# Kernel tuning notes

Measured on AMD Instinct MI355X. Metric: run time of the kernel, lower is better.

Reference implementation:

```python
import jax, jax.numpy as jnp
import numpy as np

N = 32768      # total nodes (512 graphs x 64 padded nodes)
E = 262144     # edges (avg degree 8)
F_IN = 74      # atom feature dim
D0 = 128       # dim_embedding
D1 = 256       # hidden feats
B = 512        # batch_size (graphs)
NPG = 64       # nodes per graph
EPS = 1e-5     # BatchNorm1d eps


def setup_inputs() -> dict:
    key = jax.random.key(0)
    ks = jax.random.split(key, 8)
    def rn(k, shape, s=0.05):
        return jax.random.normal(k, shape, jnp.float32) * s
    # init_transform weight [D0, F_IN]; padding=True zeroes the last row
    W_init = rn(ks[0], (D0, F_IN)).at[-1].set(0.0)
    return {
        "node_feats": jax.random.normal(ks[1], (N, F_IN), jnp.float32),
        "W_init": W_init,
        "gcn_w1": rn(ks[2], (D0, D1)), "gcn_b1": jnp.zeros((D1,), jnp.float32),
        "res_w1": rn(ks[3], (D1, D0)), "res_b1": jnp.zeros((D1,), jnp.float32),
        "bn_g1": jnp.ones((D1,), jnp.float32), "bn_b1": jnp.zeros((D1,), jnp.float32),
        "gcn_w2": rn(ks[4], (D1, D1)), "gcn_b2": jnp.zeros((D1,), jnp.float32),
        "bn_g2": jnp.ones((D1,), jnp.float32), "bn_b2": jnp.zeros((D1,), jnp.float32),
        "edge_src": jax.random.randint(ks[5], (E,), 0, N),
        "edge_dst": jax.random.randint(ks[6], (E,), 0, N),
    }


def _agg(x, src, dst):
    # DGL GraphConv norm='both': D_out^{-1/2} gather-scatter D_in^{-1/2}, degrees clamped to >= 1
    ones = jnp.ones((src.shape[0],), x.dtype)
    deg_out = jnp.clip(jax.ops.segment_sum(ones, src, num_segments=N), 1.0)
    deg_in = jnp.clip(jax.ops.segment_sum(ones, dst, num_segments=N), 1.0)
    xs = x * jax.lax.rsqrt(deg_out)[:, None]
    agg = jax.ops.segment_sum(xs[src], dst, num_segments=N)  # [N, d]
    return agg * jax.lax.rsqrt(deg_in)[:, None]


def _bn(x, g, b):
    # BatchNorm1d training-mode: batch stats over node axis, biased var
    m = x.mean(0)
    v = x.var(0)
    return (x - m) * jax.lax.rsqrt(v + EPS) * g + b


def reference(node_feats, W_init, gcn_w1, gcn_b1, res_w1, res_b1, bn_g1, bn_b1,
              gcn_w2, gcn_b2, bn_g2, bn_b2, edge_src, edge_dst):
    h = node_feats @ W_init.T  # [N, D0]
    # layer 1: residual Linear 128->256, GCN(aggregate then weight, since in<out), GELU, BN
    res = h @ res_w1.T + res_b1
    g = jax.nn.gelu(_agg(h, edge_src, edge_dst) @ gcn_w1 + gcn_b1, approximate=False)
    h = _bn(g + res, bn_g1, bn_b1)
    # layer 2: Identity residual
    g = jax.nn.gelu(_agg(h, edge_src, edge_dst) @ gcn_w2 + gcn_b2, approximate=False)
    h = _bn(g + h, bn_g2, bn_b2)
    return h.reshape(B, NPG, D1)
```

## Files before the change

### kernel.cpp

```cpp
#include <hip/hip_runtime.h>
#include <hip/hip_bf16.h>
#include <math.h>

#define N_NODES 32768
#define E_EDGES 262144
#define F_INF   74
#define KP      96
#define D0      128
#define D1      256
#define BN_EPS  1e-5f
#define RBLK    1024

#if __has_builtin(__builtin_amdgcn_cvt_pk_f32_fp8)
#define HW_FP8 1
#else
#define HW_FP8 0
#endif

typedef float f32x4 __attribute__((ext_vector_type(4)));
typedef float f32x2 __attribute__((ext_vector_type(2)));
typedef short s16x8 __attribute__((ext_vector_type(8)));

__device__ __forceinline__ float b2f(ushort h) { return __uint_as_float(((unsigned)h) << 16); }
__device__ __forceinline__ ushort f2b(float f) {
    unsigned u = __float_as_uint(f);
    return (ushort)((u + 0x7FFFu + ((u >> 16) & 1u)) >> 16);
}
__device__ __forceinline__ unsigned char f2q(float f) {
    unsigned u = __float_as_uint(f * 7.52316384526264005e-37f);
    unsigned s = (u >> 24) & 0x80u;
    int r = (int)(((u & 0x7fffffffu) + 0x80000u) >> 20);
    r = r > 126 ? 126 : r;
    return (unsigned char)(s | (unsigned)r);
}
__device__ __forceinline__ float q2f(unsigned x) {
    unsigned fb = ((x & 0x80u) << 24) | ((x & 0x7fu) << 20);
    return __uint_as_float(fb) * 1.32922799578491587e+36f;
}
__device__ __forceinline__ void acc8(float* a, uint2 v, float c) {
#if HW_FP8
    f32x2 p;
    p = __builtin_amdgcn_cvt_pk_f32_fp8((int)v.x, false); a[0] += p[0] * c; a[1] += p[1] * c;
    p = __builtin_amdgcn_cvt_pk_f32_fp8((int)v.x, true);  a[2] += p[0] * c; a[3] += p[1] * c;
    p = __builtin_amdgcn_cvt_pk_f32_fp8((int)v.y, false); a[4] += p[0] * c; a[5] += p[1] * c;
    p = __builtin_amdgcn_cvt_pk_f32_fp8((int)v.y, true);  a[6] += p[0] * c; a[7] += p[1] * c;
#else
    unsigned d;
    d = v.x; a[0] += q2f(d & 255u) * c; a[1] += q2f((d >> 8) & 255u) * c;
             a[2] += q2f((d >> 16) & 255u) * c; a[3] += q2f(d >> 24) * c;
    d = v.y; a[4] += q2f(d & 255u) * c; a[5] += q2f((d >> 8) & 255u) * c;
             a[6] += q2f((d >> 16) & 255u) * c; a[7] += q2f(d >> 24) * c;
#endif
}
__device__ __forceinline__ float gelu_exact(float x) {
    return 0.5f * x * (1.0f + erff(x * 0.70710678118654752440f));
}


__global__ void k_front_a(const int* __restrict__ src, const int* __restrict__ dst,
                          int* __restrict__ deg,
                          const float* __restrict__ nf, const float* __restrict__ Wi,
                          const float* __restrict__ w1, const float* __restrict__ rw,
                          const float* __restrict__ w2,
                          ushort* __restrict__ nfB, ushort* __restrict__ WTB,
                          ushort* __restrict__ WB1, ushort* __restrict__ RWB,
                          ushort* __restrict__ WB2) {
    int bid = blockIdx.x;
    int tid = threadIdx.x;
    if (bid < 1024) {
        int e = bid * 256 + tid;
        atomicAdd(&deg[src[e]], 1);
        atomicAdd(&deg[N_NODES + dst[e]], 1);
        return;
    }
    int idx = (bid - 1024) * 256 + tid;
    {
        int n = idx / KP, k = idx - n * KP;
        nfB[idx] = (k < F_INF) ? f2b(nf[n * F_INF + k]) : (ushort)0;
    }
    if (idx < D0 * KP) {
        int c = idx / KP, k = idx - c * KP;
        WTB[idx] = (k < F_INF) ? f2b(Wi[c * F_INF + k]) : (ushort)0;
    }
    if (idx < D1 * D0) {
        int n = idx >> 7, k = idx & 127;
        WB1[idx] = f2b(w1[k * D1 + n]);
        RWB[idx] = f2b(rw[idx]);
    }
    if (idx < D1 * D1) {
        int n = idx >> 8, k = idx & 255;
        WB2[idx] = f2b(w2[k * D1 + n]);
    }
}

__global__ __launch_bounds__(1024) void k_scan(const int* __restrict__ deg,
                                               int* __restrict__ row_off,
                                               float* __restrict__ rsq_out,
                                               float* __restrict__ rsq_in,
                                               int* __restrict__ cursor) {
    __shared__ int part[1024];
    int t = threadIdx.x;
    int base = t * 32;
    int loc[32];
    int s = 0;
    #pragma unroll
    for (int i = 0; i < 32; i++) { loc[i] = s; s += deg[N_NODES + base + i]; }
    part[t] = s;
    #pragma unroll
    for (int i = 0; i < 32; i++) {
        int n = base + i;
        int d_o = deg[n];           if (d_o < 1) d_o = 1;
        int d_i = deg[N_NODES + n]; if (d_i < 1) d_i = 1;
        rsq_out[n] = 1.0f / sqrtf((float)d_o);
        rsq_in[n]  = 1.0f / sqrtf((float)d_i);
        cursor[n] = 0;
    }
    __syncthreads();
    for (int off = 1; off < 1024; off <<= 1) {
        int v = 0;
        if (t >= off) v = part[t - off];
        __syncthreads();
        if (t >= off) part[t] += v;
        __syncthreads();
    }
    int pre = (t == 0) ? 0 : part[t - 1];
    #pragma unroll
    for (int i = 0; i < 32; i++) row_off[base + i] = pre + loc[i];
    if (t == 1023) row_off[N_NODES] = part[1023];
}


__global__ __launch_bounds__(512) void k_front_b(
    const int* __restrict__ src, const int* __restrict__ dst,
    const int* __restrict__ row_off, const float* __restrict__ rsq_out,
    int* __restrict__ cursor, int2* __restrict__ csr,
    const ushort* __restrict__ nfB, const ushort* __restrict__ WTB,
    ushort* __restrict__ h0) {
    int bid = blockIdx.x;
    int tid = threadIdx.x;
    if (bid < 512) {
        int e = bid * 512 + tid;
        int d = dst[e];
        int s = src[e];
        int slot = atomicAdd(&cursor[d], 1);
        int pos = row_off[d] + slot;
        csr[pos] = make_int2(s, __float_as_int(rsq_out[s]));
        return;
    }
    int b2 = bid - 512;
    int w = tid >> 6, lane = tid & 63, m = lane & 15, g4 = lane >> 4;
    int col = w * 16 + m;
    int rbase = b2 * 16;
    s16x8 B[3], A[3];
    #pragma unroll
    for (int j = 0; j < 3; j++)
        B[j] = *reinterpret_cast<const s16x8*>(&WTB[(size_t)col * KP + j * 32 + g4 * 8]);
    #pragma unroll
    for (int j = 0; j < 3; j++)
        A[j] = *reinterpret_cast<const s16x8*>(&nfB[(size_t)(rbase + m) * KP + j * 32 + g4 * 8]);
    f32x4 acc = (f32x4){0.f, 0.f, 0.f, 0.f};
    #pragma unroll
    for (int j = 0; j < 3; j++)
        acc = __builtin_amdgcn_mfma_f32_16x16x32_bf16(A[j], B[j], acc, 0, 0, 0);
    #pragma unroll
    for (int r = 0; r < 4; r++)
        h0[(size_t)(rbase + g4 * 4 + r) * D0 + col] = f2b(acc[r]);
}


__global__ __launch_bounds__(512) void k_layer1f(
    const ushort* __restrict__ h0B, const float* __restrict__ rsq_in,
    const int* __restrict__ row_off, const int2* __restrict__ csr,
    const ushort* __restrict__ WB1, const ushort* __restrict__ RWB,
    const float* __restrict__ b1, const float* __restrict__ rb,
    ushort* __restrict__ t1B, unsigned char* __restrict__ t1Q,
    float* __restrict__ partials) {
    __shared__ ushort sA[32 * 128];
    int tid = threadIdx.x;
    int rbase = blockIdx.x * 32;
    {
        int nloc = tid >> 4;
        int half = (tid >> 3) & 1;
        int node = rbase + nloc;
        int f = (tid & 7) * 8;
        int beg = row_off[node], end = row_off[node + 1];
        float a0[8], a1[8];
        #pragma unroll
        for (int j = 0; j < 8; j++) { a0[j] = 0.f; a1[j] = 0.f; }
        int e = beg + half;
        for (; e + 6 < end; e += 8) {
            int2 r0 = csr[e], r1 = csr[e + 2], r2 = csr[e + 4], r3 = csr[e + 6];
            float c0 = __int_as_float(r0.y), c1 = __int_as_float(r1.y);
            float c2 = __int_as_float(r2.y), c3 = __int_as_float(r3.y);
            s16x8 v00 = *reinterpret_cast<const s16x8*>(&h0B[(size_t)r0.x * D0 + f]);
            s16x8 v01 = *reinterpret_cast<const s16x8*>(&h0B[(size_t)r0.x * D0 + f + 64]);
            s16x8 v10 = *reinterpret_cast<const s16x8*>(&h0B[(size_t)r1.x * D0 + f]);
            s16x8 v11 = *reinterpret_cast<const s16x8*>(&h0B[(size_t)r1.x * D0 + f + 64]);
            s16x8 v20 = *reinterpret_cast<const s16x8*>(&h0B[(size_t)r2.x * D0 + f]);
            s16x8 v21 = *reinterpret_cast<const s16x8*>(&h0B[(size_t)r2.x * D0 + f + 64]);
            s16x8 v30 = *reinterpret_cast<const s16x8*>(&h0B[(size_t)r3.x * D0 + f]);
            s16x8 v31 = *reinterpret_cast<const s16x8*>(&h0B[(size_t)r3.x * D0 + f + 64]);
            #pragma unroll
            for (int j = 0; j < 8; j++) {
                a0[j] += b2f((ushort)v00[j]) * c0 + b2f((ushort)v10[j]) * c1 +
                         b2f((ushort)v20[j]) * c2 + b2f((ushort)v30[j]) * c3;
                a1[j] += b2f((ushort)v01[j]) * c0 + b2f((ushort)v11[j]) * c1 +
                         b2f((ushort)v21[j]) * c2 + b2f((ushort)v31[j]) * c3;
            }
        }
        for (; e < end; e += 2) {
            int2 r = csr[e];
            float sc = __int_as_float(r.y);
            s16x8 v0 = *reinterpret_cast<const s16x8*>(&h0B[(size_t)r.x * D0 + f]);
            s16x8 v1 = *reinterpret_cast<const s16x8*>(&h0B[(size_t)r.x * D0 + f + 64]);
            #pragma unroll
            for (int j = 0; j < 8; j++) {
                a0[j] += b2f((ushort)v0[j]) * sc;
                a1[j] += b2f((ushort)v1[j]) * sc;
            }
        }
        #pragma unroll
        for (int j = 0; j < 8; j++) {
            a0[j] += __shfl_xor(a0[j], 8);
            a1[j] += __shfl_xor(a1[j], 8);
        }
        if (half == 0) {
            float si = rsq_in[node];
            s16x8 o0, o1;
            #pragma unroll
            for (int j = 0; j < 8; j++) {
                o0[j] = (short)f2b(a0[j] * si);
                o1[j] = (short)f2b(a1[j] * si);
            }
            int swz = (nloc & 15) << 4;
            int x0 = f * 2;
            *reinterpret_cast<s16x8*>(((char*)sA) + nloc * 256 + (x0 ^ swz)) = o0;
            *reinterpret_cast<s16x8*>(((char*)sA) + nloc * 256 + ((x0 + 128) ^ swz)) = o1;
        }
    }
    __syncthreads();
    int w = tid >> 6, lane = tid & 63, m = lane & 15, g4 = lane >> 4;
    int cb = w * 32;
    s16x8 BG[2][4], BR[2][4];
    #pragma unroll
    for (int nt = 0; nt < 2; nt++)
        #pragma unroll
        for (int j = 0; j < 4; j++) {
            BG[nt][j] = *reinterpret_cast<const s16x8*>(&WB1[(size_t)(cb + nt * 16 + m) * D0 + j * 32 + g4 * 8]);
            BR[nt][j] = *reinterpret_cast<const s16x8*>(&RWB[(size_t)(cb + nt * 16 + m) * D0 + j * 32 + g4 * 8]);
        }
    float bg[2], brv[2];
    #pragma unroll
    for (int nt = 0; nt < 2; nt++) {
        bg[nt]  = b1[cb + nt * 16 + m];
        brv[nt] = rb[cb + nt * 16 + m];
    }
    float ps[2] = {0.f, 0.f}, pq[2] = {0.f, 0.f};
    #pragma unroll
    for (int rt = 0; rt < 2; rt++) {
        int row = rt * 16 + m;
        s16x8 aA[4], aH[4];
        #pragma unroll
        for (int j = 0; j < 4; j++) {
            int boff = row * 256 + (((j * 4 + g4) * 16) ^ ((row & 15) << 4));
            aA[j] = *reinterpret_cast<const s16x8*>(((const char*)sA) + boff);
            aH[j] = *reinterpret_cast<const s16x8*>(&h0B[(size_t)(rbase + row) * D0 + j * 32 + g4 * 8]);
        }
        f32x4 accG[2], accR[2];
        #pragma unroll
        for (int nt = 0; nt < 2; nt++) {
            accG[nt] = (f32x4){0.f, 0.f, 0.f, 0.f};
            accR[nt] = (f32x4){0.f, 0.f, 0.f, 0.f};
        }
        #pragma unroll
        for (int j = 0; j < 4; j++)
            #pragma unroll
            for (int nt = 0; nt < 2; nt++) {
                accG[nt] = __builtin_amdgcn_mfma_f32_16x16x32_bf16(aA[j], BG[nt][j], accG[nt], 0, 0, 0);
                accR[nt] = __builtin_amdgcn_mfma_f32_16x16x32_bf16(aH[j], BR[nt][j], accR[nt], 0, 0, 0);
            }
        #pragma unroll
        for (int nt = 0; nt < 2; nt++) {
            int col = cb + nt * 16 + m;
            #pragma unroll
            for (int r = 0; r < 4; r++) {
                int orow = rbase + rt * 16 + g4 * 4 + r;
                float v = gelu_exact(accG[nt][r] + bg[nt]) + accR[nt][r] + brv[nt];
                t1B[(size_t)orow * D1 + col] = f2b(v);
                t1Q[(size_t)orow * D1 + col] = f2q(v);
                ps[nt] += v; pq[nt] += v * v;
            }
        }
    }
    #pragma unroll
    for (int nt = 0; nt < 2; nt++) {
        float s = ps[nt], q = pq[nt];
        s += __shfl_xor(s, 16); s += __shfl_xor(s, 32);
        q += __shfl_xor(q, 16); q += __shfl_xor(q, 32);
        if (g4 == 0) {
            int col = cb + nt * 16 + m;
            partials[(size_t)col * RBLK + blockIdx.x] = s;
            partials[(size_t)(256 + col) * RBLK + blockIdx.x] = q;
        }
    }
}


__global__ __launch_bounds__(1024) void k_layer2f(
    const ushort* __restrict__ t1B, const unsigned char* __restrict__ t1Q,
    const float* __restrict__ sc1, const float* __restrict__ sh1,
    const float* __restrict__ rsq_in,
    const int* __restrict__ row_off, const int2* __restrict__ csr,
    const ushort* __restrict__ WB2, const float* __restrict__ b2,
    ushort* __restrict__ t2B, float* __restrict__ partials) {
    __shared__ ushort sA[32 * 256];
    int tid = threadIdx.x;
    int rbase = blockIdx.x * 32;
    {
        int nloc = tid >> 5;
        int l32 = tid & 31;
        int node = rbase + nloc;
        int f0 = l32 * 8;
        int beg = row_off[node], end = row_off[node + 1];
        int deg = end - beg;
        int grp = (tid & 63) & 32;
        float a[8];
        #pragma unroll
        for (int j = 0; j < 8; j++) a[j] = 0.f;
        float ssum = 0.f;
        int2 my = (l32 < deg) ? csr[beg + l32] : make_int2(0, 0);
        int nb = deg < 32 ? deg : 32;
        for (int kb = 0; kb < nb; kb += 8) {
            int s[8]; float c[8];
            #pragma unroll
            for (int k2 = 0; k2 < 8; k2++) {
                s[k2] = __shfl(my.x, grp + kb + k2);
                c[k2] = __int_as_float(__shfl(my.y, grp + kb + k2));
            }
            uint2 q[8];
            #pragma unroll
            for (int k2 = 0; k2 < 8; k2++)
                q[k2] = *reinterpret_cast<const uint2*>(&t1Q[(size_t)s[k2] * D1 + f0]);
            #pragma unroll
            for (int k2 = 0; k2 < 8; k2++) {
                acc8(a, q[k2], c[k2]);
                ssum += c[k2];
            }
        }
        for (int e = beg + 32; e < end; e++) {
            int2 r = csr[e];
            float sc = __int_as_float(r.y);
            uint2 q = *reinterpret_cast<const uint2*>(&t1Q[(size_t)r.x * D1 + f0]);
            ssum += sc;
            acc8(a, q, sc);
        }
        float si = rsq_in[node];
        s16x8 o;
        #pragma unroll
        for (int j = 0; j < 8; j++)
            o[j] = (short)f2b((sc1[f0 + j] * a[j] + sh1[f0 + j] * ssum) * si);
        int swz = (nloc & 15) << 4;
        int boff = nloc * 512 + ((f0 * 2) ^ swz);
        *reinterpret_cast<s16x8*>(((char*)sA) + boff) = o;
    }
    __syncthreads();
    int w = tid >> 6, lane = tid & 63, m = lane & 15, g4 = lane >> 4;
    int col = w * 16 + m;
    ushort rres[2][4];
    #pragma unroll
    for (int rt = 0; rt < 2; rt++)
        #pragma unroll
        for (int r = 0; r < 4; r++)
            rres[rt][r] = t1B[(size_t)(rbase + rt * 16 + g4 * 4 + r) * D1 + col];
    s16x8 BG[8];
    #pragma unroll
    for (int j = 0; j < 8; j++)
        BG[j] = *reinterpret_cast<const s16x8*>(&WB2[(size_t)col * D1 + j * 32 + g4 * 8]);
    float bg = b2[col], a1c = sc1[col], s1c = sh1[col];
    float ps = 0.f, pq = 0.f;
    #pragma unroll
    for (int rt = 0; rt < 2; rt++) {
        int row = rt * 16 + m;
        s16x8 aA[8];
        #pragma unroll
        for (int j = 0; j < 8; j++) {
            int boff = row * 512 + (((j * 4 + g4) * 16) ^ ((row & 15) << 4));
            aA[j] = *reinterpret_cast<const s16x8*>(((const char*)sA) + boff);
        }
        f32x4 acc = (f32x4){0.f, 0.f, 0.f, 0.f};
        #pragma unroll
        for (int j = 0; j < 8; j++)
            acc = __builtin_amdgcn_mfma_f32_16x16x32_bf16(aA[j], BG[j], acc, 0, 0, 0);
        #pragma unroll
        for (int r = 0; r < 4; r++) {
            int orow = rbase + rt * 16 + g4 * 4 + r;
            float h1v = fmaf(b2f(rres[rt][r]), a1c, s1c);
            float v = gelu_exact(acc[r] + bg) + h1v;
            t2B[(size_t)orow * D1 + col] = f2b(v);
            ps += v; pq += v * v;
        }
    }
    ps += __shfl_xor(ps, 16); ps += __shfl_xor(ps, 32);
    pq += __shfl_xor(pq, 16); pq += __shfl_xor(pq, 32);
    if (g4 == 0) {
        partials[(size_t)col * RBLK + blockIdx.x] = ps;
        partials[(size_t)(256 + col) * RBLK + blockIdx.x] = pq;
    }
}


__global__ __launch_bounds__(256) void k_reduce(
    const float* __restrict__ partials, const float* __restrict__ g,
    const float* __restrict__ b, float* __restrict__ sc, float* __restrict__ sh) {
    int c = blockIdx.x;
    int t = threadIdx.x;
    const float* ps = partials + (size_t)c * RBLK;
    const float* pq = partials + (size_t)(256 + c) * RBLK;
    float s = ps[t] + ps[t + 256] + ps[t + 512] + ps[t + 768];
    float q = pq[t] + pq[t + 256] + pq[t + 512] + pq[t + 768];
    __shared__ float Ls[256], Lq[256];
    Ls[t] = s; Lq[t] = q;
    __syncthreads();
    for (int o = 128; o > 0; o >>= 1) {
        if (t < o) { Ls[t] += Ls[t + o]; Lq[t] += Lq[t + o]; }
        __syncthreads();
    }
    if (t == 0) {
        float m = Ls[0] * (1.0f / (float)N_NODES);
        float var = Lq[0] * (1.0f / (float)N_NODES) - m * m;
        float a = g[c] / sqrtf(var + BN_EPS);
        sc[c] = a;
        sh[c] = b[c] - m * a;
    }
}


__global__ __launch_bounds__(256) void k_apply(
    const ushort* __restrict__ t2B, const float* __restrict__ sc,
    const float* __restrict__ sh, float* __restrict__ out) {
    int idx = blockIdx.x * 256 + threadIdx.x;
    size_t base = (size_t)idx * 8;
    int c = (int)(base & 255);
    s16x8 v = *reinterpret_cast<const s16x8*>(&t2B[base]);
    float4 o0, o1;
    o0.x = fmaf(b2f((ushort)v[0]), sc[c + 0], sh[c + 0]);
    o0.y = fmaf(b2f((ushort)v[1]), sc[c + 1], sh[c + 1]);
    o0.z = fmaf(b2f((ushort)v[2]), sc[c + 2], sh[c + 2]);
    o0.w = fmaf(b2f((ushort)v[3]), sc[c + 3], sh[c + 3]);
    o1.x = fmaf(b2f((ushort)v[4]), sc[c + 4], sh[c + 4]);
    o1.y = fmaf(b2f((ushort)v[5]), sc[c + 5], sh[c + 5]);
    o1.z = fmaf(b2f((ushort)v[6]), sc[c + 6], sh[c + 6]);
    o1.w = fmaf(b2f((ushort)v[7]), sc[c + 7], sh[c + 7]);
    *reinterpret_cast<float4*>(&out[base]) = o0;
    *reinterpret_cast<float4*>(&out[base + 4]) = o1;
}


static inline size_t align256(size_t x) { return (x + 255) & ~(size_t)255; }

extern "C" void kernel_launch(void* const* d_in, const int* in_sizes, int n_in,
                              void* d_out, int out_size, void* d_ws, size_t ws_size,
                              hipStream_t stream) {
    const float* node_feats = (const float*)d_in[0];
    const float* W_init     = (const float*)d_in[1];
    const float* gcn_w1     = (const float*)d_in[2];
    const float* gcn_b1     = (const float*)d_in[3];
    const float* res_w1     = (const float*)d_in[4];
    const float* res_b1     = (const float*)d_in[5];
    const float* bn_g1      = (const float*)d_in[6];
    const float* bn_b1      = (const float*)d_in[7];
    const float* gcn_w2     = (const float*)d_in[8];
    const float* gcn_b2     = (const float*)d_in[9];
    const float* bn_g2      = (const float*)d_in[10];
    const float* bn_b2      = (const float*)d_in[11];
    const int*   edge_src   = (const int*)d_in[12];
    const int*   edge_dst   = (const int*)d_in[13];
    float* out = (float*)d_out;

    char* p = (char*)d_ws;
    size_t off = 0;
    auto take = [&](size_t bytes) { void* r = p + off; off += align256(bytes); return r; };

    ushort* h0B   = (ushort*)take((size_t)N_NODES * D0 * 2);
    ushort* t1B   = (ushort*)take((size_t)N_NODES * D1 * 2);
    unsigned char* t1Q = (unsigned char*)take((size_t)N_NODES * D1);
    ushort* t2B   = (ushort*)take((size_t)N_NODES * D1 * 2);
    ushort* nfB   = (ushort*)take((size_t)N_NODES * KP * 2);
    ushort* WTB   = (ushort*)take((size_t)D0 * KP * 2);
    ushort* WB1   = (ushort*)take((size_t)D1 * D0 * 2);
    ushort* RWB   = (ushort*)take((size_t)D1 * D0 * 2);
    ushort* WB2   = (ushort*)take((size_t)D1 * D1 * 2);
    float*  part1 = (float*)take((size_t)2 * 256 * RBLK * 4);
    float*  part2 = (float*)take((size_t)2 * 256 * RBLK * 4);
    float*  sc1   = (float*)take(256 * 4);
    float*  sh1   = (float*)take(256 * 4);
    float*  sc2   = (float*)take(256 * 4);
    float*  sh2   = (float*)take(256 * 4);
    float*  rsq_out = (float*)take((size_t)N_NODES * 4);
    float*  rsq_in  = (float*)take((size_t)N_NODES * 4);
    int*    degi    = (int*)take((size_t)2 * N_NODES * 4);
    int*    cursor  = (int*)take((size_t)N_NODES * 4);
    int*    row_off = (int*)take((size_t)(N_NODES + 2) * 4);
    int2*   csr     = (int2*)take((size_t)E_EDGES * 8);

    hipMemsetAsync(degi, 0, (size_t)2 * N_NODES * 4, stream);

    k_front_a<<<1024 + (N_NODES * KP) / 256, 256, 0, stream>>>(
        edge_src, edge_dst, degi, node_feats, W_init, gcn_w1, res_w1, gcn_w2,
        nfB, WTB, WB1, RWB, WB2);

    k_scan<<<1, 1024, 0, stream>>>(degi, row_off, rsq_out, rsq_in, cursor);

    k_front_b<<<512 + N_NODES / 16, 512, 0, stream>>>(
        edge_src, edge_dst, row_off, rsq_out, cursor, csr, nfB, WTB, h0B);

    k_layer1f<<<RBLK, 512, 0, stream>>>(h0B, rsq_in, row_off, csr,
                                        WB1, RWB, gcn_b1, res_b1, t1B, t1Q, part1);
    k_reduce<<<256, 256, 0, stream>>>(part1, bn_g1, bn_b1, sc1, sh1);

    k_layer2f<<<RBLK, 1024, 0, stream>>>(t1B, t1Q, sc1, sh1, rsq_in, row_off, csr,
                                         WB2, gcn_b2, t2B, part2);
    k_reduce<<<256, 256, 0, stream>>>(part2, bn_g2, bn_b2, sc2, sh2);

    k_apply<<<(N_NODES * D1 / 8) / 256, 256, 0, stream>>>(t2B, sc2, sh2, out);
}
```

Baseline: 198.9 us.

## Overlap init-transform GEMM with single-block scan; split CSR fill into own kernel

Moves the h0 = node_feats @ W_init^T MFMA work out of the CSR-fill kernel and into the same launch as the single-block prefix scan. The scan runs in block 0 while the other blocks compute h0, 32 rows per 1024-thread block. This is meant to hide the latency of the serial one-block scan behind useful work. The CSR fill becomes its own small kernel, so the launch count stays the same but stage boundaries move.

```diff
diff --git a/kernel.cpp b/kernel.cpp
--- a/kernel.cpp
+++ b/kernel.cpp
@@ -93,64 +93,49 @@
     }
 }
 
-__global__ __launch_bounds__(1024) void k_scan(const int* __restrict__ deg,
-                                               int* __restrict__ row_off,
-                                               float* __restrict__ rsq_out,
-                                               float* __restrict__ rsq_in,
-                                               int* __restrict__ cursor) {
-    __shared__ int part[1024];
-    int t = threadIdx.x;
-    int base = t * 32;
-    int loc[32];
-    int s = 0;
-    #pragma unroll
-    for (int i = 0; i < 32; i++) { loc[i] = s; s += deg[N_NODES + base + i]; }
-    part[t] = s;
-    #pragma unroll
-    for (int i = 0; i < 32; i++) {
-        int n = base + i;
-        int d_o = deg[n];           if (d_o < 1) d_o = 1;
-        int d_i = deg[N_NODES + n]; if (d_i < 1) d_i = 1;
-        rsq_out[n] = 1.0f / sqrtf((float)d_o);
-        rsq_in[n]  = 1.0f / sqrtf((float)d_i);
-        cursor[n] = 0;
-    }
-    __syncthreads();
-    for (int off = 1; off < 1024; off <<= 1) {
-        int v = 0;
-        if (t >= off) v = part[t - off];
-        __syncthreads();
-        if (t >= off) part[t] += v;
-        __syncthreads();
-    }
-    int pre = (t == 0) ? 0 : part[t - 1];
-    #pragma unroll
-    for (int i = 0; i < 32; i++) row_off[base + i] = pre + loc[i];
-    if (t == 1023) row_off[N_NODES] = part[1023];
-}
-
-
-__global__ __launch_bounds__(512) void k_front_b(
-    const int* __restrict__ src, const int* __restrict__ dst,
-    const int* __restrict__ row_off, const float* __restrict__ rsq_out,
-    int* __restrict__ cursor, int2* __restrict__ csr,
+
+__global__ __launch_bounds__(1024) void k_scan_init(
+    const int* __restrict__ deg,
+    int* __restrict__ row_off, float* __restrict__ rsq_out,
+    float* __restrict__ rsq_in, int* __restrict__ cursor,
     const ushort* __restrict__ nfB, const ushort* __restrict__ WTB,
     ushort* __restrict__ h0) {
-    int bid = blockIdx.x;
-    int tid = threadIdx.x;
-    if (bid < 512) {
-        int e = bid * 512 + tid;
-        int d = dst[e];
-        int s = src[e];
-        int slot = atomicAdd(&cursor[d], 1);
-        int pos = row_off[d] + slot;
-        csr[pos] = make_int2(s, __float_as_int(rsq_out[s]));
+    int t = threadIdx.x;
+    if (blockIdx.x == 0) {
+        __shared__ int part[1024];
+        int base = t * 32;
+        int loc[32];
+        int s = 0;
+        #pragma unroll
+        for (int i = 0; i < 32; i++) { loc[i] = s; s += deg[N_NODES + base + i]; }
+        part[t] = s;
+        #pragma unroll
+        for (int i = 0; i < 32; i++) {
+            int n = base + i;
+            int d_o = deg[n];           if (d_o < 1) d_o = 1;
+            int d_i = deg[N_NODES + n]; if (d_i < 1) d_i = 1;
+            rsq_out[n] = 1.0f / sqrtf((float)d_o);
+            rsq_in[n]  = 1.0f / sqrtf((float)d_i);
+            cursor[n] = 0;
+        }
+        __syncthreads();
+        for (int off = 1; off < 1024; off <<= 1) {
+            int v = 0;
+            if (t >= off) v = part[t - off];
+            __syncthreads();
+            if (t >= off) part[t] += v;
+            __syncthreads();
+        }
+        int pre = (t == 0) ? 0 : part[t - 1];
+        #pragma unroll
+        for (int i = 0; i < 32; i++) row_off[base + i] = pre + loc[i];
+        if (t == 1023) row_off[N_NODES] = part[1023];
         return;
     }
-    int b2 = bid - 512;
-    int w = tid >> 6, lane = tid & 63, m = lane & 15, g4 = lane >> 4;
-    int col = w * 16 + m;
-    int rbase = b2 * 16;
+    int b2 = blockIdx.x - 1;
+    int w = t >> 6, lane = t & 63, m = lane & 15, g4 = lane >> 4;
+    int col = (w & 7) * 16 + m;
+    int rbase = b2 * 32 + (w >> 3) * 16;
     s16x8 B[3], A[3];
     #pragma unroll
     for (int j = 0; j < 3; j++)
@@ -165,6 +150,19 @@
     #pragma unroll
     for (int r = 0; r < 4; r++)
         h0[(size_t)(rbase + g4 * 4 + r) * D0 + col] = f2b(acc[r]);
+}
+
+
+__global__ __launch_bounds__(512) void k_fill(
+    const int* __restrict__ src, const int* __restrict__ dst,
+    const int* __restrict__ row_off, const float* __restrict__ rsq_out,
+    int* __restrict__ cursor, int2* __restrict__ csr) {
+    int e = blockIdx.x * 512 + threadIdx.x;
+    int d = dst[e];
+    int s = src[e];
+    int slot = atomicAdd(&cursor[d], 1);
+    int pos = row_off[d] + slot;
+    csr[pos] = make_int2(s, __float_as_int(rsq_out[s]));
 }
 
 
@@ -509,10 +507,11 @@
         edge_src, edge_dst, degi, node_feats, W_init, gcn_w1, res_w1, gcn_w2,
         nfB, WTB, WB1, RWB, WB2);
 
-    k_scan<<<1, 1024, 0, stream>>>(degi, row_off, rsq_out, rsq_in, cursor);
-
-    k_front_b<<<512 + N_NODES / 16, 512, 0, stream>>>(
-        edge_src, edge_dst, row_off, rsq_out, cursor, csr, nfB, WTB, h0B);
+    k_scan_init<<<1 + N_NODES / 32, 1024, 0, stream>>>(
+        degi, row_off, rsq_out, rsq_in, cursor, nfB, WTB, h0B);
+
+    k_fill<<<E_EDGES / 512, 512, 0, stream>>>(
+        edge_src, edge_dst, row_off, rsq_out, cursor, csr);
 
     k_layer1f<<<RBLK, 512, 0, stream>>>(h0B, rsq_in, row_off, csr,
                                         WB1, RWB, gcn_b1, res_b1, t1B, t1Q, part1);
```

New measurement: 195.1 us. Within noise of the previous version (-1.9%).
